# Kernel tuning notes

Hardware: AMD Instinct MI355X
Metric: run time of the kernel (lower is better)

The kernel has to match this reference:

```python
import jax, jax.numpy as jnp
import numpy as np

DIM_CAP = 16   # capsule dim
NCLS = 17      # annotation_nr
BS = 16
T = 120        # chunk_size * fps
P = 22         # players per frame graph
G = BS * T     # number of graphs = 1920
N = G * P      # nodes = 42240
C_IN = 14
CHS = [16, 32, 64, 152]  # 8m,16m,32m,76m with m=2
BN_EPS = 1e-3


def _build_graph():
    # fully-connected directed edges within each 22-node graph (no self loops)
    ii, jj = np.meshgrid(np.arange(P), np.arange(P), indexing='ij')
    mask = ii != jj
    li, lj = ii[mask], jj[mask]               # (462,)
    base = (np.arange(G) * P)[:, None]
    src = (base + li[None, :]).reshape(-1)
    dst = (base + lj[None, :]).reshape(-1)
    edge_index = np.stack([src, dst]).astype(np.int64)   # (2, E)
    batch = np.repeat(np.arange(G), P).astype(np.int64)  # (N,)
    return jnp.asarray(edge_index), jnp.asarray(batch)


def setup_inputs() -> dict:
    key = jax.random.key(0)
    ks = jax.random.split(key, 16)
    edge_index, batch = _build_graph()
    E = edge_index.shape[1]
    x = jax.random.normal(ks[0], (N, C_IN), dtype=jnp.float32)
    edge_attr = jax.random.uniform(ks[1], (E, 5), dtype=jnp.float32)
    dims = [C_IN] + CHS
    params = {}
    for i in range(4):
        s = 1.0 / np.sqrt(dims[i])
        params[f'W{i+1}'] = jax.random.normal(ks[2 + i], (dims[i], dims[i + 1]), dtype=jnp.float32) * s
        params[f'b{i+1}'] = jnp.zeros((dims[i + 1],), dtype=jnp.float32)
    c_out = DIM_CAP * NCLS  # 272
    params['conv_w'] = jax.random.normal(ks[6], (c_out, CHS[-1], 3), dtype=jnp.float32) * (1.0 / np.sqrt(CHS[-1] * 3))
    params['conv_b'] = jnp.zeros((c_out,), dtype=jnp.float32)
    params['bn_gamma'] = jnp.ones((T,), dtype=jnp.float32)
    params['bn_beta'] = jnp.zeros((T,), dtype=jnp.float32)
    return dict(x=x, edge_index=edge_index, batch=batch, edge_attr=edge_attr, **params)


def _gcn_layer(x, src, dst, w_edge, W, b):
    # PyG GCNConv: x' = D^-1/2 (A + I) D^-1/2 (x W) + b, edge weights w, self-loop weight 1
    n = x.shape[0]
    h = x @ W
    loop = jnp.arange(n)
    src_f = jnp.concatenate([src, loop])
    dst_f = jnp.concatenate([dst, loop])
    w_f = jnp.concatenate([w_edge, jnp.ones((n,), h.dtype)])
    deg = jax.ops.segment_sum(w_f, dst_f, num_segments=n)
    dinv = jnp.where(deg > 0, jax.lax.rsqrt(deg), 0.0)
    norm = dinv[src_f] * w_f * dinv[dst_f]
    out = jax.ops.segment_sum(norm[:, None] * h[src_f], dst_f, num_segments=n)
    return out + b


def reference(x, edge_index, batch, edge_attr, W1, b1, W2, b2, W3, b3, W4, b4,
              conv_w, conv_b, bn_gamma, bn_beta):
    src, dst = edge_index[0], edge_index[1]
    ew = edge_attr[:, 4]
    h = jax.nn.relu(_gcn_layer(x, src, dst, ew, W1, b1))
    h = jax.nn.relu(_gcn_layer(h, src, dst, ew, W2, b2))
    h = jax.nn.relu(_gcn_layer(h, src, dst, ew, W3, b3))
    h = jax.nn.relu(_gcn_layer(h, src, dst, ew, W4, b4))
    # global mean pool per graph -> (G, 152)
    ones = jnp.ones((h.shape[0],), h.dtype)
    cnt = jax.ops.segment_sum(ones, batch, num_segments=G)
    pooled = jax.ops.segment_sum(h, batch, num_segments=G) / jnp.clip(cnt, 1.0)[:, None]
    # (BS, T, 152) -> (BS, 152, T); conv kernel (3,1) with pad (1,1) on T
    feat = pooled.reshape(BS, T, CHS[-1]).transpose(0, 2, 1)
    conv = jax.lax.conv_general_dilated(
        feat, conv_w, window_strides=(1,), padding=[(1, 1)],
        dimension_numbers=('NCH', 'OIH', 'NCH'))
    conv = conv + conv_b[None, :, None]            # (BS, 272, T)
    caps = conv.transpose(0, 2, 1).reshape(BS, T, DIM_CAP, NCLS)
    # BatchNorm2d(num_features=T) in eval mode: running mean 0, var 1
    scale = (bn_gamma / jnp.sqrt(1.0 + BN_EPS))[None, :, None, None]
    shift = bn_beta[None, :, None, None]
    s = jax.nn.sigmoid(caps * scale + shift)
    out = jnp.sqrt(jnp.sum(jnp.square(s - 0.5), axis=2) * 4.0 / DIM_CAP)
    return out  # (BS, T, NCLS)
```

## Files before the change

kernel.cpp:

```cpp
#include <hip/hip_runtime.h>
#include <hip/hip_bf16.h>

#define GROUPS 1920
#define CH4 152
#define BXS 68
#define UTS 28
#define AS  28

template<int KR>
__device__ __forceinline__ void loadK(const float* p, float* xk) {
    if constexpr (KR == 2) {
        float2 v = *(const float2*)p; xk[0] = v.x; xk[1] = v.y;
    } else if constexpr (KR == 4) {
        float4 v = *(const float4*)p;
        xk[0] = v.x; xk[1] = v.y; xk[2] = v.z; xk[3] = v.w;
    } else {
        float4 v0 = *(const float4*)p, v1 = *(const float4*)(p + 4);
        xk[0] = v0.x; xk[1] = v0.y; xk[2] = v0.z; xk[3] = v0.w;
        xk[4] = v1.x; xk[5] = v1.y; xk[6] = v1.z; xk[7] = v1.w;
    }
}

template<int DIN, int KR>
__device__ __forceinline__ void layerA(const float* bufX, float* Ut,
                                       const float* A, int lane)
{
    constexpr int NKT = DIN / KR;
    const int kt = lane / 6, pt = lane % 6;
    if (kt < NKT) {
        const int p0 = pt * 4, k0 = kt * KR;
        float acc[KR][4];
        #pragma unroll
        for (int j = 0; j < KR; ++j)
            #pragma unroll
            for (int a = 0; a < 4; ++a) acc[j][a] = 0.f;
        #pragma unroll 2
        for (int q = 0; q < 22; ++q) {
            const float4 a4 = *(const float4*)(A + q * AS + p0);
            float xk[KR];
            loadK<KR>(bufX + q * BXS + k0, xk);
            #pragma unroll
            for (int j = 0; j < KR; ++j) {
                acc[j][0] = fmaf(xk[j], a4.x, acc[j][0]);
                acc[j][1] = fmaf(xk[j], a4.y, acc[j][1]);
                acc[j][2] = fmaf(xk[j], a4.z, acc[j][2]);
                acc[j][3] = fmaf(xk[j], a4.w, acc[j][3]);
            }
        }
        #pragma unroll
        for (int j = 0; j < KR; ++j)
            *(float4*)(Ut + (k0 + j) * UTS + p0) =
                make_float4(acc[j][0], acc[j][1], acc[j][2], acc[j][3]);
    }
}

template<int DIN, int DOUT, int CR>
__device__ __forceinline__ void layerB(const float* __restrict__ W,
                                       const float* __restrict__ B,
                                       const float* Ut, float* bufX, int lane)
{
    constexpr int NCT = DOUT / CR;
    const int ct = lane / 6, pt = lane % 6;
    if (ct < NCT) {
        const int p0 = pt * 4, c0 = ct * CR;
        float acc[CR][4];
        #pragma unroll
        for (int b = 0; b < CR; ++b) {
            const float bias = B[c0 + b];
            #pragma unroll
            for (int a = 0; a < 4; ++a) acc[b][a] = bias;
        }
        #pragma unroll 2
        for (int k = 0; k < DIN; ++k) {
            const float4 u4 = *(const float4*)(Ut + k * UTS + p0);
            float wv[CR];
            if constexpr (CR == 2) {
                float2 w2 = *(const float2*)(W + k * DOUT + c0);
                wv[0] = w2.x; wv[1] = w2.y;
            } else {
                #pragma unroll
                for (int b = 0; b < CR; b += 4) {
                    float4 w4 = *(const float4*)(W + k * DOUT + c0 + b);
                    wv[b] = w4.x; wv[b+1] = w4.y; wv[b+2] = w4.z; wv[b+3] = w4.w;
                }
            }
            #pragma unroll
            for (int b = 0; b < CR; ++b) {
                acc[b][0] = fmaf(wv[b], u4.x, acc[b][0]);
                acc[b][1] = fmaf(wv[b], u4.y, acc[b][1]);
                acc[b][2] = fmaf(wv[b], u4.z, acc[b][2]);
                acc[b][3] = fmaf(wv[b], u4.w, acc[b][3]);
            }
        }
        #pragma unroll
        for (int a = 0; a < 4; ++a) {
            float* dst = bufX + (p0 + a) * BXS + c0;
            if constexpr (CR == 2) {
                *(float2*)dst = make_float2(fmaxf(acc[0][a], 0.f), fmaxf(acc[1][a], 0.f));
            } else {
                #pragma unroll
                for (int b = 0; b < CR; b += 4)
                    *(float4*)(dst + b) =
                        make_float4(fmaxf(acc[b][a], 0.f), fmaxf(acc[b+1][a], 0.f),
                                    fmaxf(acc[b+2][a], 0.f), fmaxf(acc[b+3][a], 0.f));
            }
        }
    }
}

__global__ __launch_bounds__(64) void gcn_kernel(
    const float* __restrict__ x, const float* __restrict__ ea,
    const float* __restrict__ W1, const float* __restrict__ b1,
    const float* __restrict__ W2, const float* __restrict__ b2,
    const float* __restrict__ W3, const float* __restrict__ b3,
    const float* __restrict__ W4, const float* __restrict__ b4,
    float* __restrict__ pooledT)
{
    __shared__ __align__(16) float A[24 * AS];
    __shared__ __align__(16) float dv[24];
    __shared__ __align__(16) float bufX[24 * BXS];
    __shared__ __align__(16) float Ut[64 * UTS];

    const int lane = threadIdx.x;
    const int g = blockIdx.x;

    for (int idx = lane; idx < 24 * AS; idx += 64) {
        const int q = idx / AS, p = idx - q * AS;
        float v = 0.f;
        if (q < 22 && p < 22)
            v = (q == p) ? 1.0f : ea[((size_t)g * 462 + q * 21 + p - (p > q)) * 5 + 4];
        A[idx] = v;
    }
    for (int idx = lane; idx < 22 * 14; idx += 64) {
        const int p = idx / 14, k = idx - p * 14;
        bufX[p * BXS + k] = x[(size_t)g * (22 * 14) + idx];
    }
    __syncthreads();

    if (lane < 24) {
        float s = 0.f;
        #pragma unroll
        for (int q = 0; q < 22; ++q) s += A[q * AS + lane];
        dv[lane] = (s > 0.f) ? rsqrtf(s) : 0.f;
    }
    __syncthreads();
    for (int idx = lane; idx < 24 * AS; idx += 64) {
        const int q = idx / AS, p = idx - q * AS;
        if (p < 24) A[idx] *= dv[q] * dv[p];
    }
    __syncthreads();

    layerA<14, 2>(bufX, Ut, A, lane);            __syncthreads();
    layerB<14, 16, 2>(W1, b1, Ut, bufX, lane);   __syncthreads();
    layerA<16, 2>(bufX, Ut, A, lane);            __syncthreads();
    layerB<16, 32, 4>(W2, b2, Ut, bufX, lane);   __syncthreads();
    layerA<32, 4>(bufX, Ut, A, lane);            __syncthreads();
    layerB<32, 64, 8>(W3, b3, Ut, bufX, lane);   __syncthreads();
    layerA<64, 8>(bufX, Ut, A, lane);            __syncthreads();

    float* pscr = A;
    {
        const int ct = lane / 3, pt = lane - (lane / 3) * 3;
        if (lane < 57) {
            const int p0 = pt * 8, c0 = ct * 8;
            float acc[8][8];
            #pragma unroll
            for (int b = 0; b < 8; ++b) {
                const float bias = b4[c0 + b];
                #pragma unroll
                for (int a = 0; a < 8; ++a) acc[b][a] = bias;
            }
            #pragma unroll 2
            for (int k = 0; k < 64; ++k) {
                const float4 u0 = *(const float4*)(Ut + k * UTS + p0);
                const float4 u1 = *(const float4*)(Ut + k * UTS + p0 + 4);
                const float4 wa = *(const float4*)(W4 + k * 152 + c0);
                const float4 wb = *(const float4*)(W4 + k * 152 + c0 + 4);
                const float wv[8] = { wa.x, wa.y, wa.z, wa.w, wb.x, wb.y, wb.z, wb.w };
                #pragma unroll
                for (int b = 0; b < 8; ++b) {
                    acc[b][0] = fmaf(wv[b], u0.x, acc[b][0]);
                    acc[b][1] = fmaf(wv[b], u0.y, acc[b][1]);
                    acc[b][2] = fmaf(wv[b], u0.z, acc[b][2]);
                    acc[b][3] = fmaf(wv[b], u0.w, acc[b][3]);
                    acc[b][4] = fmaf(wv[b], u1.x, acc[b][4]);
                    acc[b][5] = fmaf(wv[b], u1.y, acc[b][5]);
                    acc[b][6] = fmaf(wv[b], u1.z, acc[b][6]);
                    acc[b][7] = fmaf(wv[b], u1.w, acc[b][7]);
                }
            }
            const int alim = (pt == 2) ? 6 : 8;
            float ps[8];
            #pragma unroll
            for (int b = 0; b < 8; ++b) {
                float s = 0.f;
                #pragma unroll
                for (int a = 0; a < 8; ++a)
                    s += (a < alim) ? fmaxf(acc[b][a], 0.f) : 0.f;
                ps[b] = s;
            }
            *(float4*)(pscr + pt * 156 + c0)     = make_float4(ps[0], ps[1], ps[2], ps[3]);
            *(float4*)(pscr + pt * 156 + c0 + 4) = make_float4(ps[4], ps[5], ps[6], ps[7]);
        }
    }
    __syncthreads();
    {
        const int b = g / 120, t = g - b * 120;
        for (int c = lane; c < 152; c += 64) {
            const float s = pscr[c] + pscr[156 + c] + pscr[312 + c];
            pooledT[((size_t)(b * 152 + c)) * 128 + 1 + t] = s * (1.0f / 22.0f);
        }
    }
}

__global__ __launch_bounds__(256) void repack_conv_w(const float* __restrict__ cw,
                                                     float* __restrict__ wT,
                                                     float* __restrict__ pT)
{
    const int idx = blockIdx.x * 256 + threadIdx.x;
    if (idx < 272 * 456) {
        const int o = idx / 456, r = idx - o * 456;
        wT[r * 272 + o] = cw[idx];
    } else {
        const int j = idx - 272 * 456;
        if (j < 16 * 152 * 8) {
            const int row = j >> 3, s = j & 7;
            const int slot = (s == 0) ? 0 : 120 + s;
            pT[(size_t)row * 128 + slot] = 0.f;
        }
    }
}

__global__ __launch_bounds__(320) void conv_caps_kernel(
    const float* __restrict__ pT, const float* __restrict__ wT,
    const float* __restrict__ cb, const float* __restrict__ gamma,
    const float* __restrict__ beta, float* __restrict__ out)
{
    __shared__ __align__(16) float s2[4 * 272];
    __shared__ float sc[4], sh[4];

    const int bx = blockIdx.x;
    const int b = bx / 30, tile = bx - b * 30;
    const int t0 = tile * 4;
    const int tid = threadIdx.x;

    if (tid < 4) {
        const int t = t0 + tid;
        sc[tid] = gamma[t] * 0.999500374688f;
        sh[tid] = beta[t];
    }
    __syncthreads();

    if (tid < 272) {
        const int o = tid;
        const float cb0 = cb[o];
        float acc[4] = { cb0, cb0, cb0, cb0 };
        const float* fb = pT + (size_t)b * 152 * 128 + t0;
        const float* wp = wT + o;
        #pragma unroll 4
        for (int i = 0; i < CH4; ++i) {
            const float4 fA = *(const float4*)(fb + i * 128);
            const float4 fB = *(const float4*)(fb + i * 128 + 4);
            const float fr[6] = { fA.x, fA.y, fA.z, fA.w, fB.x, fB.y };
            const float w0 = wp[(i * 3 + 0) * 272];
            const float w1 = wp[(i * 3 + 1) * 272];
            const float w2 = wp[(i * 3 + 2) * 272];
            #pragma unroll
            for (int tt = 0; tt < 4; ++tt)
                acc[tt] = fmaf(w0, fr[tt], fmaf(w1, fr[tt + 1], fmaf(w2, fr[tt + 2], acc[tt])));
        }
        #pragma unroll
        for (int tt = 0; tt < 4; ++tt) {
            const float z = fmaf(acc[tt], sc[tt], sh[tt]);
            const float s = 1.0f / (1.0f + __expf(-z));
            const float d = s - 0.5f;
            s2[tt * 272 + o] = d * d;
        }
    }
    __syncthreads();

    for (int e = tid; e < 4 * 17; e += 320) {
        const int tt = e / 17, n = e - tt * 17;
        float s = 0.f;
        #pragma unroll
        for (int d = 0; d < 16; ++d) s += s2[tt * 272 + d * 17 + n];
        out[((size_t)b * 120 + t0 + tt) * 17 + n] = sqrtf(s) * 0.5f;
    }
}

extern "C" void kernel_launch(void* const* d_in, const int* in_sizes, int n_in,
                              void* d_out, int out_size, void* d_ws, size_t ws_size,
                              hipStream_t stream) {
    const float* x     = (const float*)d_in[0];
    const float* ea    = (const float*)d_in[3];
    const float* W1    = (const float*)d_in[4];
    const float* b1    = (const float*)d_in[5];
    const float* W2    = (const float*)d_in[6];
    const float* b2    = (const float*)d_in[7];
    const float* W3    = (const float*)d_in[8];
    const float* b3    = (const float*)d_in[9];
    const float* W4    = (const float*)d_in[10];
    const float* b4    = (const float*)d_in[11];
    const float* cw    = (const float*)d_in[12];
    const float* cb    = (const float*)d_in[13];
    const float* gamma = (const float*)d_in[14];
    const float* beta  = (const float*)d_in[15];
    float* out = (float*)d_out;

    float* pT = (float*)d_ws;
    float* wT = pT + (size_t)16 * 152 * 128;

    hipLaunchKernelGGL(repack_conv_w, dim3((272 * 456 + 16 * 152 * 8 + 255) / 256),
                       dim3(256), 0, stream, cw, wT, pT);
    hipLaunchKernelGGL(gcn_kernel, dim3(GROUPS), dim3(64), 0, stream,
                       x, ea, W1, b1, W2, b2, W3, b3, W4, b4, pT);
    hipLaunchKernelGGL(conv_caps_kernel, dim3(16 * 30), dim3(320), 0, stream,
                       pT, wT, cb, gamma, beta, out);
}
```

Before: 171.1 us.

## Split final GCN aggregation into channel halves to shrink shared memory

The last neighbourhood aggregation (64 channels) now runs as two 32-channel halves. Each half is immediately consumed by the W4 projection into a register accumulator that persists across both halves. This halves the Ut scratch buffer, and the adjacency row stride drops from 28 to 24, cutting per-block LDS to allow more resident blocks. The change also adds a 3-waves launch-bounds hint and fuller unrolling of the aggregation and layerB loops, at the cost of extra barriers and possible register pressure.

New measurement: 169.8 us. Within noise of the previous version (-0.8%).

```diff
diff --git a/kernel.cpp b/kernel.cpp
--- a/kernel.cpp
+++ b/kernel.cpp
@@ -5,27 +5,23 @@
 #define CH4 152
 #define BXS 68
 #define UTS 28
-#define AS  28
+#define AS  24
 
 template<int KR>
 __device__ __forceinline__ void loadK(const float* p, float* xk) {
     if constexpr (KR == 2) {
         float2 v = *(const float2*)p; xk[0] = v.x; xk[1] = v.y;
-    } else if constexpr (KR == 4) {
+    } else {
         float4 v = *(const float4*)p;
         xk[0] = v.x; xk[1] = v.y; xk[2] = v.z; xk[3] = v.w;
-    } else {
-        float4 v0 = *(const float4*)p, v1 = *(const float4*)(p + 4);
-        xk[0] = v0.x; xk[1] = v0.y; xk[2] = v0.z; xk[3] = v0.w;
-        xk[4] = v1.x; xk[5] = v1.y; xk[6] = v1.z; xk[7] = v1.w;
-    }
-}
-
-template<int DIN, int KR>
+    }
+}
+
+template<int NK, int KR>
 __device__ __forceinline__ void layerA(const float* bufX, float* Ut,
-                                       const float* A, int lane)
-{
-    constexpr int NKT = DIN / KR;
+                                       const float* A, int lane, int kOff)
+{
+    constexpr int NKT = NK / KR;
     const int kt = lane / 6, pt = lane % 6;
     if (kt < NKT) {
         const int p0 = pt * 4, k0 = kt * KR;
@@ -34,11 +30,11 @@
         for (int j = 0; j < KR; ++j)
             #pragma unroll
             for (int a = 0; a < 4; ++a) acc[j][a] = 0.f;
-        #pragma unroll 2
+        #pragma unroll
         for (int q = 0; q < 22; ++q) {
             const float4 a4 = *(const float4*)(A + q * AS + p0);
             float xk[KR];
-            loadK<KR>(bufX + q * BXS + k0, xk);
+            loadK<KR>(bufX + q * BXS + kOff + k0, xk);
             #pragma unroll
             for (int j = 0; j < KR; ++j) {
                 acc[j][0] = fmaf(xk[j], a4.x, acc[j][0]);
@@ -70,7 +66,7 @@
             #pragma unroll
             for (int a = 0; a < 4; ++a) acc[b][a] = bias;
         }
-        #pragma unroll 2
+        #pragma unroll 8
         for (int k = 0; k < DIN; ++k) {
             const float4 u4 = *(const float4*)(Ut + k * UTS + p0);
             float wv[CR];
@@ -108,7 +104,7 @@
     }
 }
 
-__global__ __launch_bounds__(64) void gcn_kernel(
+__global__ __launch_bounds__(64, 3) void gcn_kernel(
     const float* __restrict__ x, const float* __restrict__ ea,
     const float* __restrict__ W1, const float* __restrict__ b1,
     const float* __restrict__ W2, const float* __restrict__ b2,
@@ -119,7 +115,7 @@
     __shared__ __align__(16) float A[24 * AS];
     __shared__ __align__(16) float dv[24];
     __shared__ __align__(16) float bufX[24 * BXS];
-    __shared__ __align__(16) float Ut[64 * UTS];
+    __shared__ __align__(16) float Ut[32 * UTS];
 
     const int lane = threadIdx.x;
     const int g = blockIdx.x;
@@ -146,36 +142,39 @@
     __syncthreads();
     for (int idx = lane; idx < 24 * AS; idx += 64) {
         const int q = idx / AS, p = idx - q * AS;
-        if (p < 24) A[idx] *= dv[q] * dv[p];
-    }
-    __syncthreads();
-
-    layerA<14, 2>(bufX, Ut, A, lane);            __syncthreads();
-    layerB<14, 16, 2>(W1, b1, Ut, bufX, lane);   __syncthreads();
-    layerA<16, 2>(bufX, Ut, A, lane);            __syncthreads();
-    layerB<16, 32, 4>(W2, b2, Ut, bufX, lane);   __syncthreads();
-    layerA<32, 4>(bufX, Ut, A, lane);            __syncthreads();
-    layerB<32, 64, 8>(W3, b3, Ut, bufX, lane);   __syncthreads();
-    layerA<64, 8>(bufX, Ut, A, lane);            __syncthreads();
-
-    float* pscr = A;
-    {
-        const int ct = lane / 3, pt = lane - (lane / 3) * 3;
+        A[idx] *= dv[q] * dv[p];
+    }
+    __syncthreads();
+
+    layerA<14, 2>(bufX, Ut, A, lane, 0);          __syncthreads();
+    layerB<14, 16, 2>(W1, b1, Ut, bufX, lane);    __syncthreads();
+    layerA<16, 2>(bufX, Ut, A, lane, 0);          __syncthreads();
+    layerB<16, 32, 4>(W2, b2, Ut, bufX, lane);    __syncthreads();
+    layerA<32, 4>(bufX, Ut, A, lane, 0);          __syncthreads();
+    layerB<32, 64, 8>(W3, b3, Ut, bufX, lane);    __syncthreads();
+
+    const int ct4 = lane / 3, pt4 = lane - (lane / 3) * 3;
+    float acc[8][8];
+    #pragma unroll
+    for (int b = 0; b < 8; ++b) {
+        const float bias = (lane < 57) ? b4[ct4 * 8 + b] : 0.f;
+        #pragma unroll
+        for (int a = 0; a < 8; ++a) acc[b][a] = bias;
+    }
+    #pragma unroll
+    for (int half = 0; half < 2; ++half) {
+        __syncthreads();
+        layerA<32, 4>(bufX, Ut, A, lane, half * 32);
+        __syncthreads();
         if (lane < 57) {
-            const int p0 = pt * 8, c0 = ct * 8;
-            float acc[8][8];
-            #pragma unroll
-            for (int b = 0; b < 8; ++b) {
-                const float bias = b4[c0 + b];
-                #pragma unroll
-                for (int a = 0; a < 8; ++a) acc[b][a] = bias;
-            }
-            #pragma unroll 2
-            for (int k = 0; k < 64; ++k) {
+            const int p0 = pt4 * 8, c0 = ct4 * 8;
+            const float* W4h = W4 + (size_t)half * 32 * 152;
+            #pragma unroll 4
+            for (int k = 0; k < 32; ++k) {
                 const float4 u0 = *(const float4*)(Ut + k * UTS + p0);
                 const float4 u1 = *(const float4*)(Ut + k * UTS + p0 + 4);
-                const float4 wa = *(const float4*)(W4 + k * 152 + c0);
-                const float4 wb = *(const float4*)(W4 + k * 152 + c0 + 4);
+                const float4 wa = *(const float4*)(W4h + k * 152 + c0);
+                const float4 wb = *(const float4*)(W4h + k * 152 + c0 + 4);
                 const float wv[8] = { wa.x, wa.y, wa.z, wa.w, wb.x, wb.y, wb.z, wb.w };
                 #pragma unroll
                 for (int b = 0; b < 8; ++b) {
@@ -189,19 +188,24 @@
                     acc[b][7] = fmaf(wv[b], u1.w, acc[b][7]);
                 }
             }
-            const int alim = (pt == 2) ? 6 : 8;
-            float ps[8];
-            #pragma unroll
-            for (int b = 0; b < 8; ++b) {
-                float s = 0.f;
-                #pragma unroll
-                for (int a = 0; a < 8; ++a)
-                    s += (a < alim) ? fmaxf(acc[b][a], 0.f) : 0.f;
-                ps[b] = s;
-            }
-            *(float4*)(pscr + pt * 156 + c0)     = make_float4(ps[0], ps[1], ps[2], ps[3]);
-            *(float4*)(pscr + pt * 156 + c0 + 4) = make_float4(ps[4], ps[5], ps[6], ps[7]);
-        }
+        }
+    }
+    __syncthreads();
+    float* pscr = A;
+    if (lane < 57) {
+        const int alim = (pt4 == 2) ? 6 : 8;
+        float ps[8];
+        #pragma unroll
+        for (int b = 0; b < 8; ++b) {
+            float s = 0.f;
+            #pragma unroll
+            for (int a = 0; a < 8; ++a)
+                s += (a < alim) ? fmaxf(acc[b][a], 0.f) : 0.f;
+            ps[b] = s;
+        }
+        const int c0 = ct4 * 8;
+        *(float4*)(pscr + pt4 * 156 + c0)     = make_float4(ps[0], ps[1], ps[2], ps[3]);
+        *(float4*)(pscr + pt4 * 156 + c0 + 4) = make_float4(ps[4], ps[5], ps[6], ps[7]);
     }
     __syncthreads();
     {
```

## Spread GCN graph work over 256 threads with smaller per-thread tiles

Applied to the files above, without the earlier changes.

Each per-graph block now uses 256 threads instead of a single 64-lane wave. The propagation, linear and final pooling stages are retiled so that every thread computes a smaller slice, such as one node row in the linear layers. The adjacency stride also shrinks to 24. The aim is to cut the serial per-thread work and register pressure and to get more waves per CU for latency hiding. In exchange, barriers now synchronise four waves, and more threads each issue narrower loads of the weights.

Result: no change. 174.3 us (+1.9%).

```diff
diff --git a/kernel.cpp b/kernel.cpp
--- a/kernel.cpp
+++ b/kernel.cpp
@@ -5,40 +5,31 @@
 #define CH4 152
 #define BXS 68
 #define UTS 28
-#define AS  28
-
-template<int KR>
-__device__ __forceinline__ void loadK(const float* p, float* xk) {
-    if constexpr (KR == 2) {
-        float2 v = *(const float2*)p; xk[0] = v.x; xk[1] = v.y;
-    } else if constexpr (KR == 4) {
-        float4 v = *(const float4*)p;
-        xk[0] = v.x; xk[1] = v.y; xk[2] = v.z; xk[3] = v.w;
-    } else {
-        float4 v0 = *(const float4*)p, v1 = *(const float4*)(p + 4);
-        xk[0] = v0.x; xk[1] = v0.y; xk[2] = v0.z; xk[3] = v0.w;
-        xk[4] = v1.x; xk[5] = v1.y; xk[6] = v1.z; xk[7] = v1.w;
-    }
-}
-
-template<int DIN, int KR>
+#define AS  24
+
+template<int NK, int KR>
 __device__ __forceinline__ void layerA(const float* bufX, float* Ut,
-                                       const float* A, int lane)
-{
-    constexpr int NKT = DIN / KR;
-    const int kt = lane / 6, pt = lane % 6;
-    if (kt < NKT) {
-        const int p0 = pt * 4, k0 = kt * KR;
+                                       const float* A, int tid)
+{
+    constexpr int NT = (NK / KR) * 6;
+    if (tid < NT) {
+        const int kt = tid / 6, pt = tid - (tid / 6) * 6;
+        const int k0 = kt * KR, p0 = pt * 4;
         float acc[KR][4];
         #pragma unroll
         for (int j = 0; j < KR; ++j)
             #pragma unroll
             for (int a = 0; a < 4; ++a) acc[j][a] = 0.f;
-        #pragma unroll 2
+        #pragma unroll
         for (int q = 0; q < 22; ++q) {
             const float4 a4 = *(const float4*)(A + q * AS + p0);
             float xk[KR];
-            loadK<KR>(bufX + q * BXS + k0, xk);
+            if constexpr (KR == 1) {
+                xk[0] = bufX[q * BXS + k0];
+            } else {
+                const float2 v = *(const float2*)(bufX + q * BXS + k0);
+                xk[0] = v.x; xk[1] = v.y;
+            }
             #pragma unroll
             for (int j = 0; j < KR; ++j) {
                 acc[j][0] = fmaf(xk[j], a4.x, acc[j][0]);
@@ -57,58 +48,37 @@
 template<int DIN, int DOUT, int CR>
 __device__ __forceinline__ void layerB(const float* __restrict__ W,
                                        const float* __restrict__ B,
-                                       const float* Ut, float* bufX, int lane)
+                                       const float* Ut, float* bufX, int tid)
 {
     constexpr int NCT = DOUT / CR;
-    const int ct = lane / 6, pt = lane % 6;
-    if (ct < NCT) {
-        const int p0 = pt * 4, c0 = ct * CR;
-        float acc[CR][4];
-        #pragma unroll
-        for (int b = 0; b < CR; ++b) {
-            const float bias = B[c0 + b];
-            #pragma unroll
-            for (int a = 0; a < 4; ++a) acc[b][a] = bias;
-        }
+    constexpr int NT = 24 * NCT;
+    if (tid < NT) {
+        const int p = tid / NCT, ct = tid - (tid / NCT) * NCT;
+        const int c0 = ct * CR;
+        float acc[CR];
+        #pragma unroll
+        for (int b = 0; b < CR; ++b) acc[b] = B[c0 + b];
         #pragma unroll 2
         for (int k = 0; k < DIN; ++k) {
-            const float4 u4 = *(const float4*)(Ut + k * UTS + p0);
+            const float u = Ut[k * UTS + p];
             float wv[CR];
-            if constexpr (CR == 2) {
-                float2 w2 = *(const float2*)(W + k * DOUT + c0);
-                wv[0] = w2.x; wv[1] = w2.y;
-            } else {
-                #pragma unroll
-                for (int b = 0; b < CR; b += 4) {
-                    float4 w4 = *(const float4*)(W + k * DOUT + c0 + b);
-                    wv[b] = w4.x; wv[b+1] = w4.y; wv[b+2] = w4.z; wv[b+3] = w4.w;
-                }
-            }
-            #pragma unroll
-            for (int b = 0; b < CR; ++b) {
-                acc[b][0] = fmaf(wv[b], u4.x, acc[b][0]);
-                acc[b][1] = fmaf(wv[b], u4.y, acc[b][1]);
-                acc[b][2] = fmaf(wv[b], u4.z, acc[b][2]);
-                acc[b][3] = fmaf(wv[b], u4.w, acc[b][3]);
-            }
-        }
-        #pragma unroll
-        for (int a = 0; a < 4; ++a) {
-            float* dst = bufX + (p0 + a) * BXS + c0;
-            if constexpr (CR == 2) {
-                *(float2*)dst = make_float2(fmaxf(acc[0][a], 0.f), fmaxf(acc[1][a], 0.f));
-            } else {
-                #pragma unroll
-                for (int b = 0; b < CR; b += 4)
-                    *(float4*)(dst + b) =
-                        make_float4(fmaxf(acc[b][a], 0.f), fmaxf(acc[b+1][a], 0.f),
-                                    fmaxf(acc[b+2][a], 0.f), fmaxf(acc[b+3][a], 0.f));
-            }
-        }
-    }
-}
-
-__global__ __launch_bounds__(64) void gcn_kernel(
+            #pragma unroll
+            for (int b = 0; b < CR; b += 4) {
+                const float4 w4 = *(const float4*)(W + k * DOUT + c0 + b);
+                wv[b] = w4.x; wv[b+1] = w4.y; wv[b+2] = w4.z; wv[b+3] = w4.w;
+            }
+            #pragma unroll
+            for (int b = 0; b < CR; ++b) acc[b] = fmaf(wv[b], u, acc[b]);
+        }
+        #pragma unroll
+        for (int b = 0; b < CR; b += 4)
+            *(float4*)(bufX + p * BXS + c0 + b) =
+                make_float4(fmaxf(acc[b], 0.f), fmaxf(acc[b+1], 0.f),
+                            fmaxf(acc[b+2], 0.f), fmaxf(acc[b+3], 0.f));
+    }
+}
+
+__global__ __launch_bounds__(256, 8) void gcn_kernel(
     const float* __restrict__ x, const float* __restrict__ ea,
     const float* __restrict__ W1, const float* __restrict__ b1,
     const float* __restrict__ W2, const float* __restrict__ b2,
@@ -121,95 +91,91 @@
     __shared__ __align__(16) float bufX[24 * BXS];
     __shared__ __align__(16) float Ut[64 * UTS];
 
-    const int lane = threadIdx.x;
+    const int tid = threadIdx.x;
     const int g = blockIdx.x;
 
-    for (int idx = lane; idx < 24 * AS; idx += 64) {
+    for (int idx = tid; idx < 24 * AS; idx += 256) {
         const int q = idx / AS, p = idx - q * AS;
         float v = 0.f;
         if (q < 22 && p < 22)
             v = (q == p) ? 1.0f : ea[((size_t)g * 462 + q * 21 + p - (p > q)) * 5 + 4];
         A[idx] = v;
     }
-    for (int idx = lane; idx < 22 * 14; idx += 64) {
+    for (int idx = tid; idx < 22 * 14; idx += 256) {
         const int p = idx / 14, k = idx - p * 14;
         bufX[p * BXS + k] = x[(size_t)g * (22 * 14) + idx];
     }
     __syncthreads();
 
-    if (lane < 24) {
+    if (tid < 24) {
         float s = 0.f;
         #pragma unroll
-        for (int q = 0; q < 22; ++q) s += A[q * AS + lane];
-        dv[lane] = (s > 0.f) ? rsqrtf(s) : 0.f;
-    }
-    __syncthreads();
-    for (int idx = lane; idx < 24 * AS; idx += 64) {
+        for (int q = 0; q < 22; ++q) s += A[q * AS + tid];
+        dv[tid] = (s > 0.f) ? rsqrtf(s) : 0.f;
+    }
+    __syncthreads();
+    for (int idx = tid; idx < 24 * AS; idx += 256) {
         const int q = idx / AS, p = idx - q * AS;
-        if (p < 24) A[idx] *= dv[q] * dv[p];
-    }
-    __syncthreads();
-
-    layerA<14, 2>(bufX, Ut, A, lane);            __syncthreads();
-    layerB<14, 16, 2>(W1, b1, Ut, bufX, lane);   __syncthreads();
-    layerA<16, 2>(bufX, Ut, A, lane);            __syncthreads();
-    layerB<16, 32, 4>(W2, b2, Ut, bufX, lane);   __syncthreads();
-    layerA<32, 4>(bufX, Ut, A, lane);            __syncthreads();
-    layerB<32, 64, 8>(W3, b3, Ut, bufX, lane);   __syncthreads();
-    layerA<64, 8>(bufX, Ut, A, lane);            __syncthreads();
+        A[idx] *= dv[q] * dv[p];
+    }
+    __syncthreads();
+
+    layerA<14, 1>(bufX, Ut, A, tid);           __syncthreads();
+    layerB<14, 16, 4>(W1, b1, Ut, bufX, tid);  __syncthreads();
+    layerA<16, 1>(bufX, Ut, A, tid);           __syncthreads();
+    layerB<16, 32, 4>(W2, b2, Ut, bufX, tid);  __syncthreads();
+    layerA<32, 1>(bufX, Ut, A, tid);           __syncthreads();
+    layerB<32, 64, 8>(W3, b3, Ut, bufX, tid);  __syncthreads();
+    layerA<64, 2>(bufX, Ut, A, tid);           __syncthreads();
 
     float* pscr = A;
     {
-        const int ct = lane / 3, pt = lane - (lane / 3) * 3;
-        if (lane < 57) {
-            const int p0 = pt * 8, c0 = ct * 8;
-            float acc[8][8];
-            #pragma unroll
-            for (int b = 0; b < 8; ++b) {
-                const float bias = b4[c0 + b];
-                #pragma unroll
-                for (int a = 0; a < 8; ++a) acc[b][a] = bias;
-            }
+        const int ct = tid % 76, pt = tid / 76;
+        if (tid < 228) {
+            const int c0 = ct * 2, p0 = pt * 8;
+            float acc[2][8];
+            const float bb0 = b4[c0], bb1 = b4[c0 + 1];
+            #pragma unroll
+            for (int a = 0; a < 8; ++a) { acc[0][a] = bb0; acc[1][a] = bb1; }
             #pragma unroll 2
             for (int k = 0; k < 64; ++k) {
                 const float4 u0 = *(const float4*)(Ut + k * UTS + p0);
                 const float4 u1 = *(const float4*)(Ut + k * UTS + p0 + 4);
-                const float4 wa = *(const float4*)(W4 + k * 152 + c0);
-                const float4 wb = *(const float4*)(W4 + k * 152 + c0 + 4);
-                const float wv[8] = { wa.x, wa.y, wa.z, wa.w, wb.x, wb.y, wb.z, wb.w };
-                #pragma unroll
-                for (int b = 0; b < 8; ++b) {
-                    acc[b][0] = fmaf(wv[b], u0.x, acc[b][0]);
-                    acc[b][1] = fmaf(wv[b], u0.y, acc[b][1]);
-                    acc[b][2] = fmaf(wv[b], u0.z, acc[b][2]);
-                    acc[b][3] = fmaf(wv[b], u0.w, acc[b][3]);
-                    acc[b][4] = fmaf(wv[b], u1.x, acc[b][4]);
-                    acc[b][5] = fmaf(wv[b], u1.y, acc[b][5]);
-                    acc[b][6] = fmaf(wv[b], u1.z, acc[b][6]);
-                    acc[b][7] = fmaf(wv[b], u1.w, acc[b][7]);
+                const float2 w2 = *(const float2*)(W4 + k * 152 + c0);
+                acc[0][0] = fmaf(w2.x, u0.x, acc[0][0]);
+                acc[0][1] = fmaf(w2.x, u0.y, acc[0][1]);
+                acc[0][2] = fmaf(w2.x, u0.z, acc[0][2]);
+                acc[0][3] = fmaf(w2.x, u0.w, acc[0][3]);
+                acc[0][4] = fmaf(w2.x, u1.x, acc[0][4]);
+                acc[0][5] = fmaf(w2.x, u1.y, acc[0][5]);
+                acc[0][6] = fmaf(w2.x, u1.z, acc[0][6]);
+                acc[0][7] = fmaf(w2.x, u1.w, acc[0][7]);
+                acc[1][0] = fmaf(w2.y, u0.x, acc[1][0]);
+                acc[1][1] = fmaf(w2.y, u0.y, acc[1][1]);
+                acc[1][2] = fmaf(w2.y, u0.z, acc[1][2]);
+                acc[1][3] = fmaf(w2.y, u0.w, acc[1][3]);
+                acc[1][4] = fmaf(w2.y, u1.x, acc[1][4]);
+                acc[1][5] = fmaf(w2.y, u1.y, acc[1][5]);
+                acc[1][6] = fmaf(w2.y, u1.z, acc[1][6]);
+                acc[1][7] = fmaf(w2.y, u1.w, acc[1][7]);
+            }
+            const int alim = (pt == 2) ? 6 : 8;
+            float s0 = 0.f, s1 = 0.f;
+            #pragma unroll
+            for (int a = 0; a < 8; ++a) {
+                if (a < alim) {
+                    s0 += fmaxf(acc[0][a], 0.f);
+                    s1 += fmaxf(acc[1][a], 0.f);
                 }
             }
-            const int alim = (pt == 2) ? 6 : 8;
-            float ps[8];
-            #pragma unroll
-            for (int b = 0; b < 8; ++b) {
-                float s = 0.f;
-                #pragma unroll
-                for (int a = 0; a < 8; ++a)
-                    s += (a < alim) ? fmaxf(acc[b][a], 0.f) : 0.f;
-                ps[b] = s;
-            }
-            *(float4*)(pscr + pt * 156 + c0)     = make_float4(ps[0], ps[1], ps[2], ps[3]);
-            *(float4*)(pscr + pt * 156 + c0 + 4) = make_float4(ps[4], ps[5], ps[6], ps[7]);
-        }
-    }
-    __syncthreads();
-    {
+            *(float2*)(pscr + pt * 156 + c0) = make_float2(s0, s1);
+        }
+    }
+    __syncthreads();
+    if (tid < 152) {
         const int b = g / 120, t = g - b * 120;
-        for (int c = lane; c < 152; c += 64) {
-            const float s = pscr[c] + pscr[156 + c] + pscr[312 + c];
-            pooledT[((size_t)(b * 152 + c)) * 128 + 1 + t] = s * (1.0f / 22.0f);
-        }
+        const float s = pscr[tid] + pscr[156 + tid] + pscr[312 + tid];
+        pooledT[((size_t)(b * 152 + tid)) * 128 + 1 + t] = s * (1.0f / 22.0f);
     }
 }
 
@@ -312,7 +278,7 @@
 
     hipLaunchKernelGGL(repack_conv_w, dim3((272 * 456 + 16 * 152 * 8 + 255) / 256),
                        dim3(256), 0, stream, cw, wT, pT);
-    hipLaunchKernelGGL(gcn_kernel, dim3(GROUPS), dim3(64), 0, stream,
+    hipLaunchKernelGGL(gcn_kernel, dim3(GROUPS), dim3(256), 0, stream,
                        x, ea, W1, b1, W2, b2, W3, b3, W4, b4, pT);
     hipLaunchKernelGGL(conv_caps_kernel, dim3(16 * 30), dim3(320), 0, stream,
                        pT, wT, cb, gamma, beta, out);
```
